# Optimization experiments

Hardware: AMD Instinct MI355X
Metric: run time of the kernel (lower is better)

## Reference

```python
import jax, jax.numpy as jnp
import numpy as np

DIM = 512
HEADS = 16
WIN = (7, 7)
S = WIN[0] * WIN[1]          # 49 tokens per window
NW = 64                      # windows per image (mask dim)
B_IMG = 32
B = B_IMG * NW               # 2048 total windows
TABLE = (2 * WIN[0] - 1) * (2 * WIN[1] - 1)  # 169


def _relative_position_index():
    ch = np.arange(WIN[0]); cw = np.arange(WIN[1])
    coords = np.stack(np.meshgrid(ch, cw, indexing='ij')).reshape(2, -1)  # [2, S]
    rel = coords[:, :, None] - coords[:, None, :]                          # [2, S, S]
    rel = rel.transpose(1, 2, 0).astype(np.int32)
    rel[:, :, 0] += WIN[0] - 1
    rel[:, :, 1] += WIN[1] - 1
    rel[:, :, 0] *= 2 * WIN[1] - 1
    return rel.sum(-1)  # [S, S], values in [0, TABLE)


def setup_inputs() -> dict:
    key = jax.random.key(0)
    ks = jax.random.split(key, 7)
    return {
        'x': jax.random.normal(ks[0], (B, S, DIM), jnp.float32),
        'mask': jax.random.normal(ks[1], (NW, S, S), jnp.float32),
        'qkv_w': jax.random.normal(ks[2], (DIM, 3 * DIM), jnp.float32) * (DIM ** -0.5),
        'qkv_b': jax.random.normal(ks[3], (3 * DIM,), jnp.float32) * 0.02,
        'proj_w': jax.random.normal(ks[4], (DIM, DIM), jnp.float32) * (DIM ** -0.5),
        'proj_b': jax.random.normal(ks[5], (DIM,), jnp.float32) * 0.02,
        'bias_table': jax.random.normal(ks[6], (TABLE, HEADS), jnp.float32) * 0.02,
        'rel_idx': jnp.asarray(_relative_position_index()),
    }


def reference(x, mask, qkv_w, qkv_b, proj_w, proj_b, bias_table, rel_idx):
    b, s, c = x.shape
    hd = c // HEADS
    scale = hd ** -0.5
    qkv = x @ qkv_w + qkv_b                                   # [B, S, 3C]
    qkv = qkv.reshape(b, s, 3, HEADS, hd).transpose(2, 0, 3, 1, 4)
    q, k, v = qkv[0], qkv[1], qkv[2]                          # [B, H, S, hd]
    attn = jnp.einsum('bhqd,bhkd->bhqk', q * scale, k)        # [B, H, S, S]
    # gathered relative position bias: [S*S, H] -> [H, S, S]
    bias = bias_table[rel_idx.reshape(-1)].reshape(s, s, HEADS).transpose(2, 0, 1)
    attn = attn + bias[None]
    # shifted-window mask add
    nw = mask.shape[0]
    attn = attn.reshape(-1, nw, HEADS, s, s) + mask[None, :, None]
    attn = attn.reshape(-1, HEADS, s, s)
    attn = jax.nn.softmax(attn, axis=-1)
    out = jnp.einsum('bhqk,bhkd->bhqd', attn, v)              # [B, H, S, hd]
    out = out.transpose(0, 2, 1, 3).reshape(b, s, c)
    return out @ proj_w + proj_b
```

## Files before the change

### kernel.cpp

```cpp
#include <hip/hip_runtime.h>


typedef unsigned short u16;
typedef __attribute__((ext_vector_type(8))) short short8;
typedef __attribute__((ext_vector_type(4))) float floatx4;

#define B_WIN 2048
#define SEQ 49
#define DIM 512
#define NHEAD 16
#define HD 32
#define MROWS (B_WIN * SEQ)
#define QTOT 51380224u
#define VOFF 102760448u

__device__ __forceinline__ u16 f2bf(float x) {
    unsigned u = __float_as_uint(x);
    u += 0x7fffu + ((u >> 16) & 1u);
    return (u16)(u >> 16);
}

__device__ __forceinline__ void async_ld16(const void* g, void* l) {
    __builtin_amdgcn_global_load_lds(
        (const __attribute__((address_space(1))) void*)g,
        (__attribute__((address_space(3))) void*)l, 16, 0, 0);
}

__global__ void conv_f32_bf16(const float* __restrict__ in, u16* __restrict__ out, int n4) {
    int id = blockIdx.x * 256 + threadIdx.x;
    if (id >= n4) return;
    float4 v = ((const float4*)in)[id];
    uint2 o;
    o.x = (unsigned)f2bf(v.x) | ((unsigned)f2bf(v.y) << 16);
    o.y = (unsigned)f2bf(v.z) | ((unsigned)f2bf(v.w) << 16);
    *(uint2*)(out + (size_t)id * 4) = o;
}

__global__ void transpose_conv(const float* __restrict__ in, u16* __restrict__ out, int Cn) {
    int id = blockIdx.x * 256 + threadIdx.x;
    if (id >= Cn * 512) return;
    int k = id & 511;
    int n = id >> 9;
    out[id] = f2bf(in[(size_t)k * Cn + n]);
}

__global__ void build_combined(const float* __restrict__ mask, const float* __restrict__ bias_table,
                               const int* __restrict__ rel_idx, float* __restrict__ cmb) {
    int id = blockIdx.x * 256 + threadIdx.x;
    if (id >= 64 * 16 * 49 * 64) return;
    int w64 = id & 63;
    int j   = w64 & 3;
    int l   = w64 >> 2;
    int c   = j * 16 + l;
    int t   = id >> 6;
    int row = t % 49;
    int wh  = t / 49;
    int h = wh & 15, w = wh >> 4;
    float v = -1.0e30f;
    if (c < 49) {
        int ij = row * 49 + c;
        v = bias_table[rel_idx[ij] * NHEAD + h] + mask[(size_t)w * 2401 + ij];
    }
    cmb[id] = v;
}

__global__ void zero_vpad(u16* __restrict__ qkvp) {
    int id = blockIdx.x * 256 + threadIdx.x;
    if (id >= 2048 * 16 * 32) return;
    uint4 z = {0u, 0u, 0u, 0u};
    u16* p = qkvp + VOFF + (size_t)id * 64 + 48;
    *(uint4*)p = z;
    *((uint4*)p + 1) = z;
}

__global__ __launch_bounds__(256, 2)
void gemm_qkv(const u16* __restrict__ A, const u16* __restrict__ Bt,
              const float* __restrict__ bias, u16* __restrict__ qkvp) {
    const int K = 512;
    const int tid  = threadIdx.x;
    const int lane = tid & 63, wave = tid >> 6;
    const int quad = lane >> 4, l16 = lane & 15;
    const int wr = wave >> 1, wc = wave & 1;

    const int flat = blockIdx.y * 12 + blockIdx.x;
    const int swz  = (flat & 7) * 1176 + (flat >> 3);
    const int bx = swz % 12;
    const int by = swz / 12;
    const int m0 = by * 128, n0 = bx * 128;

    __shared__ u16 smem[128 * 136];
    u16* As = smem;
    u16* Bs = smem + 4096;

    const int f0 = (wave * 2 + 0) * 512 + lane * 8;
    const int f1 = (wave * 2 + 1) * 512 + lane * 8;
    const int r0 = f0 >> 5, c0 = f0 & 31;
    const int r1 = f1 >> 5, c1 = f1 & 31;
    const u16* Ab = A + (size_t)m0 * K;
    const u16* Bb = Bt + (size_t)n0 * K;

    floatx4 acc[4][4] = {};

    for (int kt = 0; kt < K; kt += 32) {
        async_ld16(Ab + (size_t)r0 * K + kt + c0, &As[f0]);
        async_ld16(Ab + (size_t)r1 * K + kt + c1, &As[f1]);
        async_ld16(Bb + (size_t)r0 * K + kt + c0, &Bs[f0]);
        async_ld16(Bb + (size_t)r1 * K + kt + c1, &Bs[f1]);
        __syncthreads();
        short8 af[4], bf[4];
#pragma unroll
        for (int i = 0; i < 4; ++i)
            af[i] = *(const short8*)&As[(wr * 64 + i * 16 + l16) * 32 + quad * 8];
#pragma unroll
        for (int j = 0; j < 4; ++j)
            bf[j] = *(const short8*)&Bs[(wc * 64 + j * 16 + l16) * 32 + quad * 8];
#pragma unroll
        for (int i = 0; i < 4; ++i)
#pragma unroll
            for (int j = 0; j < 4; ++j)
                acc[i][j] = __builtin_amdgcn_mfma_f32_16x16x32_bf16(af[i], bf[j], acc[i][j], 0, 0, 0);
        __syncthreads();
    }

#pragma unroll
    for (int j = 0; j < 4; ++j) {
        const int col = wc * 64 + j * 16 + l16;
        const float bv = bias[n0 + col];
#pragma unroll
        for (int i = 0; i < 4; ++i)
#pragma unroll
            for (int r = 0; r < 4; ++r) {
                const int row = wr * 64 + i * 16 + quad * 4 + r;
                smem[row * 136 + col] = f2bf(acc[i][j][r] + bv);
            }
    }
    __syncthreads();

    if (n0 < 1024) {
        const int c   = n0 >> 9;
        const int hh0 = (n0 & 511) >> 5;
        u16* base = qkvp + (size_t)c * QTOT;
#pragma unroll
        for (int it = 0; it < 8; ++it) {
            const int idx  = it * 256 + tid;
            const int row  = idx >> 4;
            const int hb   = (idx >> 2) & 3;
            const int part = idx & 3;
            short8 v = *(const short8*)&smem[row * 136 + hb * 32 + part * 8];
            const int rg = m0 + row;
            const int b2 = (int)((unsigned)rg / 49u);
            const int s  = rg - b2 * 49;
            *(short8*)(base + (size_t)(b2 * 16 + hh0 + hb) * 1568 + s * 32 + part * 8) = v;
        }
    } else {
        const int hh0 = (n0 - 1024) >> 5;
        u16* base = qkvp + VOFF;
#pragma unroll 16
        for (int it = 0; it < 64; ++it) {
            const int idx = it * 256 + tid;
            const int col = idx >> 7;
            const int row = idx & 127;
            const u16 v = smem[row * 136 + col];
            const int rg = m0 + row;
            const int b2 = (int)((unsigned)rg / 49u);
            const int s  = rg - b2 * 49;
            const int hh = hh0 + (col >> 5);
            const int d  = col & 31;
            base[(size_t)(b2 * 16 + hh) * 2048 + d * 64 + s] = v;
        }
    }
}

__global__ __launch_bounds__(256, 2)
void gemm_bt(const u16* __restrict__ A, const u16* __restrict__ Bt,
             const float* __restrict__ bias, float* __restrict__ Cout,
             int M, int N, int K) {
    const int tid  = threadIdx.x;
    const int lane = tid & 63, wave = tid >> 6;
    const int quad = lane >> 4, l16 = lane & 15;
    const int wr = wave >> 1, wc = wave & 1;

    const int nbx = gridDim.x, nby = gridDim.y;
    const int total = nbx * nby;
    const int flat = blockIdx.y * nbx + blockIdx.x;
    const int swz = ((total & 7) == 0) ? ((flat & 7) * (total >> 3) + (flat >> 3)) : flat;
    const int bx = swz % nbx;
    const int by = swz / nbx;
    const int m0 = by * 128, n0 = bx * 128;

    __shared__ u16 As[128 * 32];
    __shared__ u16 Bs[128 * 32];

    const int f0 = (wave * 2 + 0) * 512 + lane * 8;
    const int f1 = (wave * 2 + 1) * 512 + lane * 8;
    const int r0 = f0 >> 5, c0 = f0 & 31;
    const int r1 = f1 >> 5, c1 = f1 & 31;
    const u16* Ab = A + (size_t)m0 * K;
    const u16* Bb = Bt + (size_t)n0 * K;

    floatx4 acc[4][4] = {};

    for (int kt = 0; kt < K; kt += 32) {
        async_ld16(Ab + (size_t)r0 * K + kt + c0, &As[f0]);
        async_ld16(Ab + (size_t)r1 * K + kt + c1, &As[f1]);
        async_ld16(Bb + (size_t)r0 * K + kt + c0, &Bs[f0]);
        async_ld16(Bb + (size_t)r1 * K + kt + c1, &Bs[f1]);
        __syncthreads();
        short8 af[4], bf[4];
#pragma unroll
        for (int i = 0; i < 4; ++i)
            af[i] = *(const short8*)&As[(wr * 64 + i * 16 + l16) * 32 + quad * 8];
#pragma unroll
        for (int j = 0; j < 4; ++j)
            bf[j] = *(const short8*)&Bs[(wc * 64 + j * 16 + l16) * 32 + quad * 8];
#pragma unroll
        for (int i = 0; i < 4; ++i)
#pragma unroll
            for (int j = 0; j < 4; ++j)
                acc[i][j] = __builtin_amdgcn_mfma_f32_16x16x32_bf16(af[i], bf[j], acc[i][j], 0, 0, 0);
        __syncthreads();
    }

#pragma unroll
    for (int i = 0; i < 4; ++i) {
#pragma unroll
        for (int j = 0; j < 4; ++j) {
            int col = n0 + wc * 64 + j * 16 + l16;
            float bv = bias[col];
#pragma unroll
            for (int r = 0; r < 4; ++r) {
                int row = m0 + wr * 64 + i * 16 + quad * 4 + r;
                Cout[(size_t)row * N + col] = acc[i][j][r] + bv;
            }
        }
    }
}

__global__ __launch_bounds__(64, 4)
void attn2(const u16* __restrict__ qkvp, const float* __restrict__ cmbp,
           u16* __restrict__ out) {
    const int lane = threadIdx.x;
    const int quad = lane >> 4, l16 = lane & 15;
    const int p0 = blockIdx.x * 2;
    const int b  = p0 >> 4, h0 = p0 & 15;

    const u16* qb0 = qkvp + (size_t)p0 * 1568;
    const u16* kb0 = qb0 + QTOT;
    const u16* qb1 = qb0 + 1568;
    const u16* kb1 = kb0 + 1568;
    const u16* vb0 = qkvp + VOFF + (size_t)p0 * 2048;
    const u16* vb1 = vb0 + 2048;

    const float* cb0 = cmbp + (size_t)(((b & 63) * 16 + h0) * 49) * 64;
    const float* cb1 = cb0 + 49 * 64;

    u16* op0 = out + (size_t)b * SEQ * DIM + h0 * HD;
    u16* op1 = op0 + HD;

    __shared__ u16 ps[64 * 72];

    int rr[4];
#pragma unroll
    for (int i = 0; i < 4; ++i) { int r = i * 16 + l16; rr[i] = r > 48 ? 48 : r; }

    short8 af0[4], bf0[4], af1[4], bf1[4];
#pragma unroll
    for (int i = 0; i < 4; ++i) af0[i] = *(const short8*)(qb0 + rr[i] * 32 + quad * 8);
#pragma unroll
    for (int j = 0; j < 4; ++j) bf0[j] = *(const short8*)(kb0 + rr[j] * 32 + quad * 8);
#pragma unroll
    for (int i = 0; i < 4; ++i) af1[i] = *(const short8*)(qb1 + rr[i] * 32 + quad * 8);
#pragma unroll
    for (int j = 0; j < 4; ++j) bf1[j] = *(const short8*)(kb1 + rr[j] * 32 + quad * 8);

    const float scale = 0.1767766952966369f;

    auto do_pair = [&](const short8* af, const short8* bfr, const float* cb,
                       const u16* vb, u16* op) {
        short8 vf[2][2];
#pragma unroll
        for (int kt = 0; kt < 2; ++kt)
#pragma unroll
            for (int jn = 0; jn < 2; ++jn)
                vf[kt][jn] = *(const short8*)(vb + (jn * 16 + l16) * 64 + kt * 32 + quad * 8);

#pragma unroll
        for (int i = 0; i < 4; ++i) {
            floatx4 accS[4] = {};
#pragma unroll
            for (int j = 0; j < 4; ++j)
                accS[j] = __builtin_amdgcn_mfma_f32_16x16x32_bf16(af[i], bfr[j], accS[j], 0, 0, 0);
            const int rbase = i * 16 + quad * 4;
#pragma unroll
            for (int r = 0; r < 4; ++r) {
                const int row = rbase + r;
                const int rc = row < 48 ? row : 48;
                float4 c4 = *(const float4*)(cb + rc * 64 + l16 * 4);
                float x[4] = { accS[0][r] * scale + c4.x, accS[1][r] * scale + c4.y,
                               accS[2][r] * scale + c4.z, accS[3][r] * scale + c4.w };
                float m = fmaxf(fmaxf(x[0], x[1]), fmaxf(x[2], x[3]));
#pragma unroll
                for (int off = 1; off < 16; off <<= 1) m = fmaxf(m, __shfl_xor(m, off));
                float e[4], s = 0.f;
#pragma unroll
                for (int j = 0; j < 4; ++j) { e[j] = __expf(x[j] - m); s += e[j]; }
#pragma unroll
                for (int off = 1; off < 16; off <<= 1) s += __shfl_xor(s, off);
                float inv = __builtin_amdgcn_rcpf(s);
#pragma unroll
                for (int j = 0; j < 4; ++j)
                    ps[row * 72 + j * 16 + l16] = f2bf(e[j] * inv);
            }
        }
        __syncthreads();

        floatx4 accO[4][2] = {};
#pragma unroll
        for (int kt = 0; kt < 2; ++kt) {
            short8 pf[4];
#pragma unroll
            for (int i = 0; i < 4; ++i)
                pf[i] = *(const short8*)&ps[(i * 16 + l16) * 72 + kt * 32 + quad * 8];
#pragma unroll
            for (int i = 0; i < 4; ++i)
#pragma unroll
                for (int jn = 0; jn < 2; ++jn)
                    accO[i][jn] = __builtin_amdgcn_mfma_f32_16x16x32_bf16(pf[i], vf[kt][jn], accO[i][jn], 0, 0, 0);
        }
        __syncthreads();

#pragma unroll
        for (int i = 0; i < 4; ++i)
#pragma unroll
            for (int jn = 0; jn < 2; ++jn)
#pragma unroll
                for (int r = 0; r < 4; ++r) {
                    int row = i * 16 + quad * 4 + r;
                    if (row < SEQ)
                        op[(size_t)row * DIM + jn * 16 + l16] = f2bf(accO[i][jn][r]);
                }
    };

    do_pair(af0, bf0, cb0, vb0, op0);
    do_pair(af1, bf1, cb1, vb1, op1);
}

extern "C" void kernel_launch(void* const* d_in, const int* in_sizes, int n_in,
                              void* d_out, int out_size, void* d_ws, size_t ws_size,
                              hipStream_t stream) {
    const float* x         = (const float*)d_in[0];
    const float* mask      = (const float*)d_in[1];
    const float* qkv_w     = (const float*)d_in[2];
    const float* qkv_b     = (const float*)d_in[3];
    const float* proj_w    = (const float*)d_in[4];
    const float* proj_b    = (const float*)d_in[5];
    const float* bias_tab  = (const float*)d_in[6];
    const int*   rel_idx   = (const int*)d_in[7];
    float* out = (float*)d_out;

    char* ws = (char*)d_ws;
    u16*   xbf     = (u16*)(ws + 0);
    u16*   qkvp    = (u16*)(ws + 102760448);
    u16*   wqkv_t  = (u16*)(ws + 452333568);
    u16*   wproj_t = (u16*)(ws + 453906432);
    float* cmb     = out;

    conv_f32_bf16<<<50176, 256, 0, stream>>>(x, xbf, 12845056);
    transpose_conv<<<3072, 256, 0, stream>>>(qkv_w, wqkv_t, 1536);
    transpose_conv<<<1024, 256, 0, stream>>>(proj_w, wproj_t, 512);
    build_combined<<<12544, 256, 0, stream>>>(mask, bias_tab, rel_idx, cmb);
    zero_vpad<<<4096, 256, 0, stream>>>(qkvp);
    gemm_qkv<<<dim3(12, 784), 256, 0, stream>>>(xbf, wqkv_t, qkv_b, qkvp);
    attn2<<<B_WIN * NHEAD / 2, 64, 0, stream>>>(qkvp, cmb, xbf);
    gemm_bt<<<dim3(4, 784), 256, 0, stream>>>(xbf, wproj_t, proj_b, out,
                                              MROWS, 512, 512);
}
```

Measured before the change: 856.2 us.

## Compute transposed scores in attention to keep softmax in registers without LDS

The attention kernel now computes S^T = K·Q^T, so each query's scores sit in one lane group. The softmax reduction then needs only two cross-lane shuffles, and the P operand for the PV MFMA is rebuilt with register shuffles instead of a round trip through shared memory and two barriers. The combined bias/mask table is stored in natural column order and pre-scaled by log2(e), so exp2 can replace exp. Outputs are packed to bf16 in registers and written at the end, which raises register pressure and adds shuffle traffic in exchange.

```diff
diff --git a/kernel.cpp b/kernel.cpp
--- a/kernel.cpp
+++ b/kernel.cpp
@@ -4,6 +4,7 @@
 typedef unsigned short u16;
 typedef __attribute__((ext_vector_type(8))) short short8;
 typedef __attribute__((ext_vector_type(4))) float floatx4;
+typedef __attribute__((ext_vector_type(4))) unsigned u32x4;
 
 #define B_WIN 2048
 #define SEQ 49
@@ -46,20 +47,18 @@
 
 __global__ void build_combined(const float* __restrict__ mask, const float* __restrict__ bias_table,
                                const int* __restrict__ rel_idx, float* __restrict__ cmb) {
+    const float LOG2E = 1.4426950408889634f;
     int id = blockIdx.x * 256 + threadIdx.x;
     if (id >= 64 * 16 * 49 * 64) return;
-    int w64 = id & 63;
-    int j   = w64 & 3;
-    int l   = w64 >> 2;
-    int c   = j * 16 + l;
+    int col = id & 63;
     int t   = id >> 6;
     int row = t % 49;
     int wh  = t / 49;
     int h = wh & 15, w = wh >> 4;
     float v = -1.0e30f;
-    if (c < 49) {
-        int ij = row * 49 + c;
-        v = bias_table[rel_idx[ij] * NHEAD + h] + mask[(size_t)w * 2401 + ij];
+    if (col < 49) {
+        int ij = row * 49 + col;
+        v = (bias_table[rel_idx[ij] * NHEAD + h] + mask[(size_t)w * 2401 + ij]) * LOG2E;
     }
     cmb[id] = v;
 }
@@ -246,103 +245,122 @@
 
     const u16* qb0 = qkvp + (size_t)p0 * 1568;
     const u16* kb0 = qb0 + QTOT;
-    const u16* qb1 = qb0 + 1568;
-    const u16* kb1 = kb0 + 1568;
     const u16* vb0 = qkvp + VOFF + (size_t)p0 * 2048;
-    const u16* vb1 = vb0 + 2048;
-
-    const float* cb0 = cmbp + (size_t)(((b & 63) * 16 + h0) * 49) * 64;
-    const float* cb1 = cb0 + 49 * 64;
+    const float* cb0 = cmbp + (size_t)((b & 63) * 16 + h0) * 49 * 64;
 
     u16* op0 = out + (size_t)b * SEQ * DIM + h0 * HD;
     u16* op1 = op0 + HD;
 
-    __shared__ u16 ps[64 * 72];
-
-    int rr[4];
-#pragma unroll
-    for (int i = 0; i < 4; ++i) { int r = i * 16 + l16; rr[i] = r > 48 ? 48 : r; }
-
-    short8 af0[4], bf0[4], af1[4], bf1[4];
-#pragma unroll
-    for (int i = 0; i < 4; ++i) af0[i] = *(const short8*)(qb0 + rr[i] * 32 + quad * 8);
-#pragma unroll
-    for (int j = 0; j < 4; ++j) bf0[j] = *(const short8*)(kb0 + rr[j] * 32 + quad * 8);
-#pragma unroll
-    for (int i = 0; i < 4; ++i) af1[i] = *(const short8*)(qb1 + rr[i] * 32 + quad * 8);
-#pragma unroll
-    for (int j = 0; j < 4; ++j) bf1[j] = *(const short8*)(kb1 + rr[j] * 32 + quad * 8);
-
-    const float scale = 0.1767766952966369f;
-
-    auto do_pair = [&](const short8* af, const short8* bfr, const float* cb,
-                       const u16* vb, u16* op) {
+    const float scale2 = 0.2550348754f;
+
+    unsigned ob0[4][2][2], ob1[4][2][2];
+
+    auto run_pair = [&](const u16* qb, const u16* kb, const u16* vb,
+                        const float* cbp, unsigned (&ob)[4][2][2]) {
+        short8 kf[4];
+#pragma unroll
+        for (int i = 0; i < 4; ++i) {
+            int rk = i * 16 + l16; if (rk > 48) rk = 48;
+            kf[i] = *(const short8*)(kb + rk * 32 + quad * 8);
+        }
         short8 vf[2][2];
 #pragma unroll
         for (int kt = 0; kt < 2; ++kt)
 #pragma unroll
-            for (int jn = 0; jn < 2; ++jn)
-                vf[kt][jn] = *(const short8*)(vb + (jn * 16 + l16) * 64 + kt * 32 + quad * 8);
-
-#pragma unroll
-        for (int i = 0; i < 4; ++i) {
-            floatx4 accS[4] = {};
-#pragma unroll
-            for (int j = 0; j < 4; ++j)
-                accS[j] = __builtin_amdgcn_mfma_f32_16x16x32_bf16(af[i], bfr[j], accS[j], 0, 0, 0);
-            const int rbase = i * 16 + quad * 4;
-#pragma unroll
-            for (int r = 0; r < 4; ++r) {
-                const int row = rbase + r;
-                const int rc = row < 48 ? row : 48;
-                float4 c4 = *(const float4*)(cb + rc * 64 + l16 * 4);
-                float x[4] = { accS[0][r] * scale + c4.x, accS[1][r] * scale + c4.y,
-                               accS[2][r] * scale + c4.z, accS[3][r] * scale + c4.w };
-                float m = fmaxf(fmaxf(x[0], x[1]), fmaxf(x[2], x[3]));
-#pragma unroll
-                for (int off = 1; off < 16; off <<= 1) m = fmaxf(m, __shfl_xor(m, off));
-                float e[4], s = 0.f;
-#pragma unroll
-                for (int j = 0; j < 4; ++j) { e[j] = __expf(x[j] - m); s += e[j]; }
-#pragma unroll
-                for (int off = 1; off < 16; off <<= 1) s += __shfl_xor(s, off);
-                float inv = __builtin_amdgcn_rcpf(s);
-#pragma unroll
-                for (int j = 0; j < 4; ++j)
-                    ps[row * 72 + j * 16 + l16] = f2bf(e[j] * inv);
-            }
-        }
-        __syncthreads();
-
-        floatx4 accO[4][2] = {};
-#pragma unroll
-        for (int kt = 0; kt < 2; ++kt) {
-            short8 pf[4];
+            for (int n = 0; n < 2; ++n)
+                vf[kt][n] = *(const short8*)(vb + (n * 16 + l16) * 64 + kt * 32 + quad * 8);
+
+#pragma unroll
+        for (int j = 0; j < 4; ++j) {
+            const int q  = j * 16 + l16;
+            const int rc = q < 49 ? q : 48;
+            const short8 qf = *(const short8*)(qb + rc * 32 + quad * 8);
+
+            floatx4 accT[4] = {};
 #pragma unroll
             for (int i = 0; i < 4; ++i)
-                pf[i] = *(const short8*)&ps[(i * 16 + l16) * 72 + kt * 32 + quad * 8];
+                accT[i] = __builtin_amdgcn_mfma_f32_16x16x32_bf16(kf[i], qf, accT[i], 0, 0, 0);
+
+            float x[4][4];
+            float m = -3.0e38f;
+#pragma unroll
+            for (int i = 0; i < 4; ++i) {
+                float4 c4 = *(const float4*)(cbp + rc * 64 + i * 16 + quad * 4);
+                x[i][0] = accT[i][0] * scale2 + c4.x;
+                x[i][1] = accT[i][1] * scale2 + c4.y;
+                x[i][2] = accT[i][2] * scale2 + c4.z;
+                x[i][3] = accT[i][3] * scale2 + c4.w;
+                m = fmaxf(m, fmaxf(fmaxf(x[i][0], x[i][1]), fmaxf(x[i][2], x[i][3])));
+            }
+            m = fmaxf(m, __shfl_xor(m, 16));
+            m = fmaxf(m, __shfl_xor(m, 32));
+
+            float s = 0.f;
 #pragma unroll
             for (int i = 0; i < 4; ++i)
 #pragma unroll
-                for (int jn = 0; jn < 2; ++jn)
-                    accO[i][jn] = __builtin_amdgcn_mfma_f32_16x16x32_bf16(pf[i], vf[kt][jn], accO[i][jn], 0, 0, 0);
-        }
-        __syncthreads();
-
-#pragma unroll
-        for (int i = 0; i < 4; ++i)
-#pragma unroll
-            for (int jn = 0; jn < 2; ++jn)
-#pragma unroll
                 for (int r = 0; r < 4; ++r) {
-                    int row = i * 16 + quad * 4 + r;
-                    if (row < SEQ)
-                        op[(size_t)row * DIM + jn * 16 + l16] = f2bf(accO[i][jn][r]);
+                    float e = __builtin_amdgcn_exp2f(x[i][r] - m);
+                    x[i][r] = e; s += e;
                 }
+            s += __shfl_xor(s, 16);
+            s += __shfl_xor(s, 32);
+            const float inv = __builtin_amdgcn_rcpf(s);
+
+            unsigned pk[4][2];
+#pragma unroll
+            for (int i = 0; i < 4; ++i) {
+                pk[i][0] = (unsigned)f2bf(x[i][0] * inv) | ((unsigned)f2bf(x[i][1] * inv) << 16);
+                pk[i][1] = (unsigned)f2bf(x[i][2] * inv) | ((unsigned)f2bf(x[i][3] * inv) << 16);
+            }
+
+            floatx4 accO[2] = {};
+#pragma unroll
+            for (int kt = 0; kt < 2; ++kt) {
+                u32x4 w;
+#pragma unroll
+                for (int W = 0; W < 4; ++W) {
+                    const int src = (((quad & 1) * 2 + (W >> 1)) << 4) + l16;
+                    const unsigned lo = (unsigned)__shfl((int)pk[2 * kt + 0][W & 1], src);
+                    const unsigned hi = (unsigned)__shfl((int)pk[2 * kt + 1][W & 1], src);
+                    w[W] = (quad & 2) ? hi : lo;
+                }
+                const short8 pa = __builtin_bit_cast(short8, w);
+#pragma unroll
+                for (int n = 0; n < 2; ++n)
+                    accO[n] = __builtin_amdgcn_mfma_f32_16x16x32_bf16(pa, vf[kt][n], accO[n], 0, 0, 0);
+            }
+#pragma unroll
+            for (int n = 0; n < 2; ++n) {
+                ob[j][n][0] = (unsigned)f2bf(accO[n][0]) | ((unsigned)f2bf(accO[n][1]) << 16);
+                ob[j][n][1] = (unsigned)f2bf(accO[n][2]) | ((unsigned)f2bf(accO[n][3]) << 16);
+            }
+        }
     };
 
-    do_pair(af0, bf0, cb0, vb0, op0);
-    do_pair(af1, bf1, cb1, vb1, op1);
+    run_pair(qb0,        kb0,        vb0,        cb0,           ob0);
+    run_pair(qb0 + 1568, kb0 + 1568, vb0 + 2048, cb0 + 49 * 64, ob1);
+
+#pragma unroll
+    for (int j = 0; j < 4; ++j)
+#pragma unroll
+        for (int r = 0; r < 4; ++r) {
+            const int row = j * 16 + quad * 4 + r;
+            if (row < SEQ) {
+#pragma unroll
+                for (int n = 0; n < 2; ++n) {
+                    const unsigned w = ob0[j][n][r >> 1];
+                    op0[(size_t)row * DIM + n * 16 + l16] =
+                        (u16)((r & 1) ? (w >> 16) : (w & 0xffffu));
+                }
+#pragma unroll
+                for (int n = 0; n < 2; ++n) {
+                    const unsigned w = ob1[j][n][r >> 1];
+                    op1[(size_t)row * DIM + n * 16 + l16] =
+                        (u16)((r & 1) ? (w >> 16) : (w & 0xffffu));
+                }
+            }
+        }
 }
 
 extern "C" void kernel_launch(void* const* d_in, const int* in_sizes, int n_in,
```

Result: no change. 855.2 us (-0.1%).
